# Kernel tuning notes

Hardware: AMD Instinct MI355X
Metric: run time of the kernel (lower is better)

## Reference

```python
import jax, jax.numpy as jnp
import numpy as np

B, T, D, E, K = 4, 2048, 1024, 8, 2

def setup_inputs() -> dict:
    key = jax.random.key(0)
    ks = jax.random.split(key, 4)
    scale = 1.0 / np.sqrt(D)
    return {
        "input_feat": jax.random.normal(ks[0], (B, T, D), dtype=jnp.float32),
        "delta": jax.random.normal(ks[1], (B, T, D), dtype=jnp.float32),
        "gate_W": jax.random.normal(ks[2], (E, D), dtype=jnp.float32) * scale,
        "gate_b": jnp.zeros((E,), dtype=jnp.float32),
        "expert_W": jax.random.normal(ks[3], (E, D, D), dtype=jnp.float32) * scale,
        "expert_b": jnp.zeros((E, D), dtype=jnp.float32),
    }

def reference(input_feat, delta, gate_W, gate_b, expert_W, expert_b):
    # Gating: logits [B,T,E], top-k over experts, softmax over the k logits
    gate_logits = jnp.einsum("btd,ed->bte", input_feat, gate_W) + gate_b
    topk_vals, topk_idx = jax.lax.top_k(gate_logits, K)          # [B,T,K]
    topk_weights = jax.nn.softmax(topk_vals, axis=-1)            # [B,T,K]

    # Dense per-expert linear on delta: [B,T,D,E] (torch Linear: x @ W.T + b)
    expert_outputs = jnp.einsum("btd,efd->btfe", delta, expert_W) + expert_b.T

    # Gather top-k expert outputs and weighted-combine
    idx = jnp.broadcast_to(topk_idx[:, :, None, :], (B, T, D, K))
    topk_outputs = jnp.take_along_axis(expert_outputs, idx, axis=-1)  # [B,T,D,K]
    weighted_output = jnp.sum(topk_outputs * topk_weights[:, :, None, :], axis=-1)
    return weighted_output
```

## Files before the change

### kernel.cpp

```cpp
#include <hip/hip_runtime.h>
#include <hip/hip_fp16.h>
#include <stdint.h>

#define NTOK 8192
#define D 1024
#define E 8
#define BM 128
#define BN 64
#define BK 64
#define GEMM_GRID ((NTOK / BM) * (D / BN) * E)

typedef __attribute__((ext_vector_type(8))) short short8;
typedef __attribute__((ext_vector_type(4))) float f32x4;

__device__ __forceinline__ ushort f2bf(float f) {
  uint32_t x = __float_as_uint(f);
  x += 0x7FFFu + ((x >> 16) & 1u);
  return (ushort)(x >> 16);
}

__device__ __forceinline__ ushort f2h(float f) {
  union { __half h; ushort u; } cv;
  cv.h = __float2half(f);
  return cv.u;
}
__device__ __forceinline__ float h2f(ushort u) {
  union { __half h; ushort u; } cv;
  cv.u = u;
  return __half2float(cv.h);
}

#define NW4 2097152
#define ND4 2097152
__global__ __launch_bounds__(256) void convert_kernel(
    const float* __restrict__ expert_W, const float* __restrict__ delta,
    ushort* __restrict__ Wb, ushort* __restrict__ Db, int* __restrict__ cnt) {
  int i = blockIdx.x * 256 + threadIdx.x;
  if (i < E) cnt[i] = 0;
  if (i < NW4) {
    float4 v = ((const float4*)expert_W)[i];
    ushort4 u; u.x = f2bf(v.x); u.y = f2bf(v.y); u.z = f2bf(v.z); u.w = f2bf(v.w);
    ((ushort4*)Wb)[i] = u;
  } else {
    int j = i - NW4;
    float4 v = ((const float4*)delta)[j];
    ushort4 u; u.x = f2bf(v.x); u.y = f2bf(v.y); u.z = f2bf(v.z); u.w = f2bf(v.w);
    ((ushort4*)Db)[j] = u;
  }
}

__global__ __launch_bounds__(256) void gatebin_kernel(
    const float* __restrict__ x, const float* __restrict__ gW,
    const float* __restrict__ gb, int* __restrict__ cnt,
    int* __restrict__ list, float* __restrict__ wlist) {
  int wv = threadIdx.x >> 6;
  int lane = threadIdx.x & 63;
  int tid = threadIdx.x;
  int t = blockIdx.x * 4 + wv;

  const float4* xr = (const float4*)(x + (size_t)t * D) + lane * 4;
  float acc[E];
#pragma unroll
  for (int e = 0; e < E; ++e) acc[e] = 0.f;
#pragma unroll
  for (int qq = 0; qq < 4; ++qq) {
    float4 xv = xr[qq];
#pragma unroll
    for (int e = 0; e < E; ++e) {
      float4 wvv = ((const float4*)(gW + e * D))[lane * 4 + qq];
      acc[e] += xv.x * wvv.x + xv.y * wvv.y + xv.z * wvv.z + xv.w * wvv.w;
    }
  }
#pragma unroll
  for (int e = 0; e < E; ++e) {
    float v = acc[e];
#pragma unroll
    for (int off = 32; off > 0; off >>= 1) v += __shfl_xor(v, off, 64);
    acc[e] = v;
  }

  __shared__ int sIdx[4];
  __shared__ float2 sW[4];
  __shared__ int hist[E];
  __shared__ int base[E];
  __shared__ int rofs[4][2];

  if (lane == 0) {
    float lg[E];
#pragma unroll
    for (int e = 0; e < E; ++e) lg[e] = acc[e] + gb[e];
    int i0 = 0; float v0 = lg[0];
#pragma unroll
    for (int e = 1; e < E; ++e) { if (lg[e] > v0) { v0 = lg[e]; i0 = e; } }
    int i1 = -1; float v1 = -1e30f;
#pragma unroll
    for (int e = 0; e < E; ++e) { if (e != i0 && lg[e] > v1) { v1 = lg[e]; i1 = e; } }
    float e1 = __expf(v1 - v0);
    float inv = 1.f / (1.f + e1);
    sIdx[wv] = i0 | (i1 << 16);
    sW[wv] = make_float2(inv, e1 * inv);
  }
  if (tid < E) hist[tid] = 0;
  __syncthreads();

  if (tid == 0) {
#pragma unroll
    for (int w4 = 0; w4 < 4; ++w4) {
      int p = sIdx[w4];
      rofs[w4][0] = hist[p & 0xFFFF]++;
      rofs[w4][1] = hist[p >> 16]++;
    }
  }
  __syncthreads();
  if (tid < E) base[tid] = hist[tid] ? atomicAdd(&cnt[tid], hist[tid]) : 0;
  __syncthreads();

  if (tid == 0) {
#pragma unroll
    for (int w4 = 0; w4 < 4; ++w4) {
      int p = sIdx[w4];
      int tk = blockIdx.x * 4 + w4;
      int e0 = p & 0xFFFF, e1 = p >> 16;
      int s0 = base[e0] + rofs[w4][0];
      list[e0 * NTOK + s0] = tk;
      wlist[e0 * NTOK + s0] = sW[w4].x;
      int s1 = base[e1] + rofs[w4][1];
      list[e1 * NTOK + s1] = tk | 0x80000000;
      wlist[e1 * NTOK + s1] = sW[w4].y;
    }
  }
}

__global__ __launch_bounds__(256) void moe_gemm_kernel(
    const ushort* __restrict__ Db, const ushort* __restrict__ Wb,
    const float* __restrict__ eb, const int* __restrict__ cnt,
    const int* __restrict__ list, const float* __restrict__ wlist,
    float* __restrict__ out) {
  const int bx = blockIdx.x;
  const int e  = bx & 7;
  const int mn = bx >> 3;
  const int mt = mn >> 4;
  const int nt = mn & 15;
  const int M  = cnt[e];
  const int m0 = mt * BM;
  if (m0 >= M) return;
  const int n0 = nt * BN;

  __shared__ ushort As[BM * BK];
  __shared__ ushort Bs[BN * BK];

  const int tid = threadIdx.x;
  const int wv = tid >> 6;
  const int lane = tid & 63;
  const int wm = wv >> 1;
  const int wn = wv & 1;
  const int c = lane & 15;
  const int q = lane >> 4;

  const int* listE = list + e * NTOK;

  const int rloc = lane >> 3;
  const int gglob = (lane & 7) ^ rloc;
  const ushort* aptr[4];
  ushort* alds[4];
#pragma unroll
  for (int p = 0; p < 4; ++p) {
    int r = m0 + wv * 32 + p * 8 + rloc;
    int tok = listE[r < M ? r : m0] & 0x7FFFFFFF;
    aptr[p] = Db + (size_t)tok * D + gglob * 8;
    alds[p] = &As[(wv * 32 + p * 8) * BK];
  }
  const ushort* WbE = Wb + ((size_t)e << 20);
  const ushort* bptr[2];
  ushort* blds[2];
#pragma unroll
  for (int sub = 0; sub < 2; ++sub) {
    int row = n0 + wv * 16 + sub * 8 + rloc;
    bptr[sub] = WbE + (size_t)row * D + gglob * 8;
    blds[sub] = &Bs[(wv * 16 + sub * 8) * BK];
  }

  f32x4 acc[4][2];
#pragma unroll
  for (int i = 0; i < 4; ++i)
#pragma unroll
    for (int j = 0; j < 2; ++j)
      acc[i][j] = (f32x4){0.f, 0.f, 0.f, 0.f};

  for (int k0 = 0; k0 < D; k0 += BK) {
#pragma unroll
    for (int p = 0; p < 4; ++p)
      __builtin_amdgcn_global_load_lds(
          (const __attribute__((address_space(1))) void*)(aptr[p] + k0),
          (__attribute__((address_space(3))) void*)alds[p], 16, 0, 0);
#pragma unroll
    for (int sub = 0; sub < 2; ++sub)
      __builtin_amdgcn_global_load_lds(
          (const __attribute__((address_space(1))) void*)(bptr[sub] + k0),
          (__attribute__((address_space(3))) void*)blds[sub], 16, 0, 0);
    __syncthreads();

#pragma unroll
    for (int s = 0; s < 2; ++s) {
      const int sw = (((s * 4 + q) ^ (c & 7)) * 8);
      short8 a[4], b[2];
#pragma unroll
      for (int i = 0; i < 4; ++i)
        a[i] = *(const short8*)&As[(wm * 64 + i * 16 + c) * BK + sw];
#pragma unroll
      for (int j = 0; j < 2; ++j)
        b[j] = *(const short8*)&Bs[(wn * 32 + j * 16 + c) * BK + sw];
#pragma unroll
      for (int i = 0; i < 4; ++i)
#pragma unroll
        for (int j = 0; j < 2; ++j)
          acc[i][j] = __builtin_amdgcn_mfma_f32_16x16x32_bf16(a[i], b[j], acc[i][j], 0, 0, 0);
    }
    __syncthreads();
  }

  float bias[2];
#pragma unroll
  for (int j = 0; j < 2; ++j)
    bias[j] = eb[e * D + n0 + wn * 32 + j * 16 + c];
  const float* wlE = wlist + e * NTOK;
  ushort* outh = (ushort*)out;
#pragma unroll
  for (int i = 0; i < 4; ++i) {
#pragma unroll
    for (int r = 0; r < 4; ++r) {
      int m = m0 + wm * 64 + i * 16 + q * 4 + r;
      if (m < M) {
        int en = listE[m];
        int tok = en & 0x7FFFFFFF;
        int rank = ((unsigned)en) >> 31;
        float w = wlE[m];
        size_t bi = ((size_t)tok * D + n0 + wn * 32 + c) * 2 + rank;
#pragma unroll
        for (int j = 0; j < 2; ++j)
          outh[bi + j * 32] = f2h((acc[i][j][r] + bias[j]) * w);
      }
    }
  }
}

#define NC4 2097152
__global__ __launch_bounds__(256) void combine_kernel(float* __restrict__ out) {
  int i = blockIdx.x * 256 + threadIdx.x;
  uint4 v = ((const uint4*)out)[i];
  float4 r;
  r.x = h2f((ushort)(v.x & 0xFFFF)) + h2f((ushort)(v.x >> 16));
  r.y = h2f((ushort)(v.y & 0xFFFF)) + h2f((ushort)(v.y >> 16));
  r.z = h2f((ushort)(v.z & 0xFFFF)) + h2f((ushort)(v.z >> 16));
  r.w = h2f((ushort)(v.w & 0xFFFF)) + h2f((ushort)(v.w >> 16));
  ((float4*)out)[i] = r;
}

extern "C" void kernel_launch(void* const* d_in, const int* in_sizes, int n_in,
                              void* d_out, int out_size, void* d_ws, size_t ws_size,
                              hipStream_t stream) {
  const float* input_feat = (const float*)d_in[0];
  const float* delta      = (const float*)d_in[1];
  const float* gate_W     = (const float*)d_in[2];
  const float* gate_b     = (const float*)d_in[3];
  const float* expert_W   = (const float*)d_in[4];
  const float* expert_b   = (const float*)d_in[5];
  float* out = (float*)d_out;

  char* ws = (char*)d_ws;
  ushort* Wb    = (ushort*)ws;
  ushort* Db    = (ushort*)(ws + 16777216);
  char*   meta  = ws + 2 * 16777216;
  int*    cnt   = (int*)meta;
  int*    list  = (int*)(meta + 256);
  float*  wlist = (float*)(meta + 256 + NTOK * E * 4);

  convert_kernel<<<(NW4 + ND4) / 256, 256, 0, stream>>>(expert_W, delta, Wb, Db, cnt);
  gatebin_kernel<<<NTOK / 4, 256, 0, stream>>>(input_feat, gate_W, gate_b, cnt, list, wlist);
  moe_gemm_kernel<<<GEMM_GRID, 256, 0, stream>>>(
      Db, Wb, expert_b, cnt, list, wlist, out);
  combine_kernel<<<NC4 / 256, 256, 0, stream>>>(out);
}
```

Before: 230.6 us.

## Double-buffer GEMM shared-memory tiles with BK=32 to overlap loads and MFMA

```diff
diff --git a/kernel.cpp b/kernel.cpp
--- a/kernel.cpp
+++ b/kernel.cpp
@@ -7,7 +7,10 @@
 #define E 8
 #define BM 128
 #define BN 64
-#define BK 64
+#define BK 32
+#define NKT (D / BK)
+#define ABUF (BM * BK)
+#define BBUF (BN * BK)
 #define GEMM_GRID ((NTOK / BM) * (D / BN) * E)
 
 typedef __attribute__((ext_vector_type(8))) short short8;
@@ -146,8 +149,8 @@
   if (m0 >= M) return;
   const int n0 = nt * BN;
 
-  __shared__ ushort As[BM * BK];
-  __shared__ ushort Bs[BN * BK];
+  __shared__ ushort As[2 * ABUF];
+  __shared__ ushort Bs[2 * BBUF];
 
   const int tid = threadIdx.x;
   const int wv = tid >> 6;
@@ -159,26 +162,22 @@
 
   const int* listE = list + e * NTOK;
 
-  const int rloc = lane >> 3;
-  const int gglob = (lane & 7) ^ rloc;
-  const ushort* aptr[4];
-  ushort* alds[4];
-#pragma unroll
-  for (int p = 0; p < 4; ++p) {
-    int r = m0 + wv * 32 + p * 8 + rloc;
+  const int rl = lane >> 2;
+  const int sl = lane & 3;
+  const int gs = sl ^ (rl & 3);
+  const ushort* aptr[2];
+  ushort* alds[2];
+#pragma unroll
+  for (int p = 0; p < 2; ++p) {
+    int r = m0 + wv * 32 + p * 16 + rl;
     int tok = listE[r < M ? r : m0] & 0x7FFFFFFF;
-    aptr[p] = Db + (size_t)tok * D + gglob * 8;
-    alds[p] = &As[(wv * 32 + p * 8) * BK];
+    aptr[p] = Db + (size_t)tok * D + gs * 8;
+    alds[p] = &As[(wv * 32 + p * 16) * BK];
   }
   const ushort* WbE = Wb + ((size_t)e << 20);
-  const ushort* bptr[2];
-  ushort* blds[2];
-#pragma unroll
-  for (int sub = 0; sub < 2; ++sub) {
-    int row = n0 + wv * 16 + sub * 8 + rloc;
-    bptr[sub] = WbE + (size_t)row * D + gglob * 8;
-    blds[sub] = &Bs[(wv * 16 + sub * 8) * BK];
-  }
+  const int brow = n0 + wv * 16 + rl;
+  const ushort* bptr = WbE + (size_t)brow * D + gs * 8;
+  ushort* blds = &Bs[(wv * 16) * BK];
 
   f32x4 acc[4][2];
 #pragma unroll
@@ -187,35 +186,48 @@
     for (int j = 0; j < 2; ++j)
       acc[i][j] = (f32x4){0.f, 0.f, 0.f, 0.f};
 
-  for (int k0 = 0; k0 < D; k0 += BK) {
-#pragma unroll
-    for (int p = 0; p < 4; ++p)
+#pragma unroll
+  for (int p = 0; p < 2; ++p)
+    __builtin_amdgcn_global_load_lds(
+        (const __attribute__((address_space(1))) void*)(aptr[p]),
+        (__attribute__((address_space(3))) void*)(alds[p]), 16, 0, 0);
+  __builtin_amdgcn_global_load_lds(
+      (const __attribute__((address_space(1))) void*)(bptr),
+      (__attribute__((address_space(3))) void*)(blds), 16, 0, 0);
+  __syncthreads();
+
+  const int swr = (q ^ (c & 3)) * 8;
+
+  for (int kt = 0; kt < NKT; ++kt) {
+    const int cur = kt & 1;
+    if (kt < NKT - 1) {
+      const int nx = cur ^ 1;
+      const int kk = (kt + 1) * BK;
+#pragma unroll
+      for (int p = 0; p < 2; ++p)
+        __builtin_amdgcn_global_load_lds(
+            (const __attribute__((address_space(1))) void*)(aptr[p] + kk),
+            (__attribute__((address_space(3))) void*)(alds[p] + nx * ABUF), 16, 0, 0);
       __builtin_amdgcn_global_load_lds(
-          (const __attribute__((address_space(1))) void*)(aptr[p] + k0),
-          (__attribute__((address_space(3))) void*)alds[p], 16, 0, 0);
-#pragma unroll
-    for (int sub = 0; sub < 2; ++sub)
-      __builtin_amdgcn_global_load_lds(
-          (const __attribute__((address_space(1))) void*)(bptr[sub] + k0),
-          (__attribute__((address_space(3))) void*)blds[sub], 16, 0, 0);
-    __syncthreads();
-
-#pragma unroll
-    for (int s = 0; s < 2; ++s) {
-      const int sw = (((s * 4 + q) ^ (c & 7)) * 8);
-      short8 a[4], b[2];
-#pragma unroll
-      for (int i = 0; i < 4; ++i)
-        a[i] = *(const short8*)&As[(wm * 64 + i * 16 + c) * BK + sw];
+          (const __attribute__((address_space(1))) void*)(bptr + kk),
+          (__attribute__((address_space(3))) void*)(blds + nx * BBUF), 16, 0, 0);
+    }
+
+    const ushort* Ab = As + cur * ABUF;
+    const ushort* Bb = Bs + cur * BBUF;
+    short8 a[4], b[2];
+#pragma unroll
+    for (int i = 0; i < 4; ++i)
+      a[i] = *(const short8*)&Ab[(wm * 64 + i * 16 + c) * BK + swr];
+#pragma unroll
+    for (int j = 0; j < 2; ++j)
+      b[j] = *(const short8*)&Bb[(wn * 32 + j * 16 + c) * BK + swr];
+#pragma unroll
+    for (int i = 0; i < 4; ++i)
 #pragma unroll
       for (int j = 0; j < 2; ++j)
-        b[j] = *(const short8*)&Bs[(wn * 32 + j * 16 + c) * BK + sw];
-#pragma unroll
-      for (int i = 0; i < 4; ++i)
-#pragma unroll
-        for (int j = 0; j < 2; ++j)
-          acc[i][j] = __builtin_amdgcn_mfma_f32_16x16x32_bf16(a[i], b[j], acc[i][j], 0, 0, 0);
-    }
+        acc[i][j] = __builtin_amdgcn_mfma_f32_16x16x32_bf16(a[i], b[j], acc[i][j], 0, 0, 0);
+
     __syncthreads();
   }
 
```

Result: slower. 242.3 us (+5.1%).
